# Kernel tuning notes

Hardware: AMD Instinct MI355X
Metric: run time of the kernel (lower is better)

## Reference

```python
import jax, jax.numpy as jnp
import numpy as np

NF, NLOC, NALL, NNEI = 2, 3072, 4096, 128
NTYPES, NSPLINE = 4, 1024
RCUT, RMIN, HH = 6.0, 0.0, 0.006
BOX = 20.0


def setup_inputs() -> dict:
    key = jax.random.key(0)
    k1, k2, k3, k4, k5 = jax.random.split(key, 5)
    extended_coord = jax.random.uniform(k1, (NF, NALL, 3), dtype=jnp.float32) * BOX
    extended_atype = jax.random.randint(k2, (NF, NALL), 0, NTYPES, dtype=jnp.int32)
    nlist = jax.random.randint(k3, (NF, NLOC, NNEI), 0, NALL, dtype=jnp.int32)
    # avoid self-neighbors (zero distance)
    self_idx = jnp.arange(NLOC, dtype=jnp.int32)[None, :, None]
    nlist = jnp.where(nlist == self_idx, (nlist + 1) % NALL, nlist)
    drop = jax.random.uniform(k4, (NF, NLOC, NNEI)) < 0.15
    nlist = jnp.where(drop, -1, nlist)
    tab_info = jnp.array([RMIN, HH, float(NSPLINE)], dtype=jnp.float32)
    tab_data = jax.random.normal(k5, (NTYPES, NTYPES, NSPLINE, 4), dtype=jnp.float32) * 0.1
    return {
        "extended_coord": extended_coord,
        "extended_atype": extended_atype,
        "nlist": nlist,
        "tab_info": tab_info,
        "tab_data": tab_data,
    }


def reference(extended_coord, extended_atype, nlist, tab_info, tab_data):
    nf, nloc, nnei = nlist.shape
    masked_nlist = jnp.clip(nlist, 0)
    # dense pairwise distances, as in the original module (nf, nall, nall)
    dr = extended_coord[:, :, None, :] - extended_coord[:, None, :, :]
    rr_full = jnp.sqrt(jnp.maximum(jnp.sum(dr * dr, axis=-1), 1e-30))
    # gather distances of listed neighbors (nf, nloc, nnei)
    rr = jnp.take_along_axis(rr_full[:, :nloc, :], masked_nlist, axis=2)
    i_type = extended_atype[:, :nloc]                                  # (nf, nloc)
    j_type = extended_atype[jnp.arange(nf)[:, None, None], masked_nlist]  # (nf, nloc, nnei)

    rmin = tab_info[0]
    hh = tab_info[1]
    uu = (rr - rmin) / hh
    uu = jnp.where(nlist != -1, uu, float(NSPLINE + 1))
    idx = uu.astype(jnp.int32)  # truncation toward zero, matches torch .to(int)
    uu = uu - idx

    # gather cubic-spline coefficients: (nf, nloc, nnei, 4)
    cidx = jnp.clip(idx, 0, NSPLINE - 1)
    coef = tab_data[i_type[:, :, None], j_type, cidx]
    coef = jnp.where((idx > NSPLINE)[..., None], 0.0, coef)

    a3, a2, a1, a0 = coef[..., 0], coef[..., 1], coef[..., 2], coef[..., 3]
    ener = ((a3 * uu + a2) * uu + a1) * uu + a0
    # zero beyond cutoff / beyond table range
    beyond = (rr >= RCUT) | (rr >= rmin + NSPLINE * hh)
    ener = jnp.where(beyond, 0.0, ener)
    # zero masked (padded) neighbor entries, then reduce over neighbors
    ener = jnp.where(nlist != -1, ener, 0.0)
    return 0.5 * jnp.sum(ener, axis=-1)  # (nf, nloc)
```

## Files before the change

kernel.cpp:

```cpp
#include <hip/hip_runtime.h>

#define NF      2
#define NLOC    3072
#define NALL    4096
#define NNEI    128
#define NTYPES  4
#define NSPLINE 1024

__device__ __forceinline__ float opaque(float x) {
    asm volatile("" : "+v"(x));
    return x;
}

__global__ __launch_bounds__(256) void pairtab_kernel(
    const float* __restrict__ coord,
    const int*   __restrict__ atype,
    const int*   __restrict__ nlist,
    const float* __restrict__ tab_info,
    const float* __restrict__ tab_data,
    float*       __restrict__ out)
{
    const int tid   = threadIdx.x;
    const int r     = tid >> 7;
    const int jj    = tid & 127;
    const int row   = blockIdx.x * 2 + r;

    const int f = (row >= NLOC) ? 1 : 0;
    const int i = row - f * NLOC;

    const float rmin = tab_info[0];
    const float hh   = tab_info[1];
    const float hi   = opaque((float)(1.0 / (double)hh));
    const float cut2 = opaque(opaque(1024.0f * hh) + rmin);

    const float* ci = coord + (size_t)(f * NALL + i) * 3;
    const float xi = ci[0], yi = ci[1], zi = ci[2];
    const int itype = atype[f * NALL + i];

    const int nj = nlist[(size_t)(f * NLOC + i) * NNEI + jj];
    const int mj = (nj < 0) ? 0 : nj;

    const float* cj = coord + (size_t)(f * NALL + mj) * 3;

    const float dx = opaque(xi - cj[0]);
    const float dy = opaque(yi - cj[1]);
    const float dz = opaque(zi - cj[2]);
    const float x2 = opaque(dx * dx);
    const float y2 = opaque(dy * dy);
    const float z2 = opaque(dz * dz);
    float ss = opaque(opaque(x2 + y2) + z2);
    ss = fmaxf(ss, 1e-30f);

    const float rr = (float)sqrt((double)ss);

    const float num = opaque(rr - rmin);
    float uu = opaque(num * hi);
    if (nj == -1) uu = (float)(NSPLINE + 1);

    const int idx = (int)uu;
    const float fu = opaque(uu - (float)idx);
    int cidx = idx;
    if (cidx < 0) cidx = 0;
    if (cidx > NSPLINE - 1) cidx = NSPLINE - 1;

    const int jtype = atype[f * NALL + mj];
    const float4 c4 = *(const float4*)(tab_data +
        ((size_t)((itype * NTYPES + jtype) * NSPLINE + cidx)) * 4);

    float a3 = c4.x, a2 = c4.y, a1 = c4.z, a0 = c4.w;
    if (idx > NSPLINE) { a3 = 0.f; a2 = 0.f; a1 = 0.f; a0 = 0.f; }

    float e = opaque(opaque(opaque(opaque(opaque(a3 * fu) + a2) * fu)
                            + a1) * fu) + a0;

    if (rr >= 6.0f || rr >= cut2 || nj == -1) e = 0.0f;

    double acc = (double)e;
    #pragma unroll
    for (int off = 32; off; off >>= 1)
        acc += __shfl_xor(acc, off);

    __shared__ double part[4];
    if ((tid & 63) == 0) part[tid >> 6] = acc;
    __syncthreads();
    if (jj == 0)
        out[row] = (float)(0.5 * (part[r * 2] + part[r * 2 + 1]));
}

extern "C" void kernel_launch(void* const* d_in, const int* in_sizes, int n_in,
                              void* d_out, int out_size, void* d_ws, size_t ws_size,
                              hipStream_t stream) {
    const float* coord    = (const float*)d_in[0];
    const int*   atype    = (const int*)  d_in[1];
    const int*   nlist    = (const int*)  d_in[2];
    const float* tab_info = (const float*)d_in[3];
    const float* tab_data = (const float*)d_in[4];
    float* out = (float*)d_out;

    const int blocks = (NF * NLOC) / 2;
    pairtab_kernel<<<blocks, 256, 0, stream>>>(coord, atype, nlist, tab_info,
                                               tab_data, out);
}
```

Measured before the change: 13.15 us.

## Stage frame coordinates and types in LDS, process eight rows per block

Each block now loads the entire frame's coordinates and atom types (4096 atoms packed as float4) into shared memory, then serves the random neighbor gathers from LDS instead of global memory. Blocks grow to 1024 threads covering 8 rows, and spline coefficient loads use nontemporal hints. The cost is that every block reloads 64KB of coordinates and types, 768 blocks in total, which adds global traffic and a full barrier before any useful work, and the large LDS footprint limits occupancy.

```diff
diff --git a/kernel.cpp b/kernel.cpp
--- a/kernel.cpp
+++ b/kernel.cpp
@@ -6,13 +6,16 @@
 #define NNEI    128
 #define NTYPES  4
 #define NSPLINE 1024
+#define RPB     8
+
+typedef float f32x4 __attribute__((ext_vector_type(4)));
 
 __device__ __forceinline__ float opaque(float x) {
     asm volatile("" : "+v"(x));
     return x;
 }
 
-__global__ __launch_bounds__(256) void pairtab_kernel(
+__global__ __launch_bounds__(1024) void pairtab_kernel(
     const float* __restrict__ coord,
     const int*   __restrict__ atype,
     const int*   __restrict__ nlist,
@@ -20,31 +23,51 @@
     const float* __restrict__ tab_data,
     float*       __restrict__ out)
 {
-    const int tid   = threadIdx.x;
-    const int r     = tid >> 7;
-    const int jj    = tid & 127;
-    const int row   = blockIdx.x * 2 + r;
+    __shared__ f32x4  atoms[NALL];
+    __shared__ double part[16];
+    float* ldsf = (float*)atoms;
 
-    const int f = (row >= NLOC) ? 1 : 0;
-    const int i = row - f * NLOC;
+    const int tid  = threadIdx.x;
+    const int row0 = blockIdx.x * RPB;
+    const int f    = (row0 >= NLOC) ? 1 : 0;
+
+    const float* cbase = coord + (size_t)f * NALL * 3;
+    #pragma unroll
+    for (int g = tid; g < NALL * 3; g += 1024) {
+        const float v = cbase[g];
+        const int a = g / 3;
+        const int comp = g - a * 3;
+        ldsf[a * 4 + comp] = v;
+    }
+    const int* tb = atype + (size_t)f * NALL;
+    #pragma unroll
+    for (int g = tid; g < NALL; g += 1024)
+        ldsf[g * 4 + 3] = __int_as_float(tb[g]);
+    __syncthreads();
+
+    const int rl   = tid >> 7;
+    const int jj   = tid & 127;
+    const int grow = row0 + rl;
+    const int i    = grow - f * NLOC;
 
     const float rmin = tab_info[0];
     const float hh   = tab_info[1];
     const float hi   = opaque((float)(1.0 / (double)hh));
     const float cut2 = opaque(opaque(1024.0f * hh) + rmin);
 
-    const float* ci = coord + (size_t)(f * NALL + i) * 3;
-    const float xi = ci[0], yi = ci[1], zi = ci[2];
-    const int itype = atype[f * NALL + i];
+    const f32x4 pi = atoms[i];
+    const float xi = pi.x, yi = pi.y, zi = pi.z;
+    const int itype = __float_as_int(pi.w);
 
-    const int nj = nlist[(size_t)(f * NLOC + i) * NNEI + jj];
+    const int nj = nlist[(size_t)grow * NNEI + jj];
     const int mj = (nj < 0) ? 0 : nj;
 
-    const float* cj = coord + (size_t)(f * NALL + mj) * 3;
+    const f32x4 pj = atoms[mj];
+    const int jtype = __float_as_int(pj.w);
 
-    const float dx = opaque(xi - cj[0]);
-    const float dy = opaque(yi - cj[1]);
-    const float dz = opaque(zi - cj[2]);
+    const float dx = opaque(xi - pj.x);
+    const float dy = opaque(yi - pj.y);
+    const float dz = opaque(zi - pj.z);
     const float x2 = opaque(dx * dx);
     const float y2 = opaque(dy * dy);
     const float z2 = opaque(dz * dz);
@@ -63,9 +86,9 @@
     if (cidx < 0) cidx = 0;
     if (cidx > NSPLINE - 1) cidx = NSPLINE - 1;
 
-    const int jtype = atype[f * NALL + mj];
-    const float4 c4 = *(const float4*)(tab_data +
-        ((size_t)((itype * NTYPES + jtype) * NSPLINE + cidx)) * 4);
+    const f32x4* tp = (const f32x4*)tab_data +
+        ((size_t)((itype * NTYPES + jtype) * NSPLINE + cidx));
+    const f32x4 c4 = __builtin_nontemporal_load(tp);
 
     float a3 = c4.x, a2 = c4.y, a1 = c4.z, a0 = c4.w;
     if (idx > NSPLINE) { a3 = 0.f; a2 = 0.f; a1 = 0.f; a0 = 0.f; }
@@ -80,11 +103,10 @@
     for (int off = 32; off; off >>= 1)
         acc += __shfl_xor(acc, off);
 
-    __shared__ double part[4];
     if ((tid & 63) == 0) part[tid >> 6] = acc;
     __syncthreads();
     if (jj == 0)
-        out[row] = (float)(0.5 * (part[r * 2] + part[r * 2 + 1]));
+        out[grow] = (float)(0.5 * (part[rl * 2] + part[rl * 2 + 1]));
 }
 
 extern "C" void kernel_launch(void* const* d_in, const int* in_sizes, int n_in,
@@ -97,7 +119,7 @@
     const float* tab_data = (const float*)d_in[4];
     float* out = (float*)d_out;
 
-    const int blocks = (NF * NLOC) / 2;
-    pairtab_kernel<<<blocks, 256, 0, stream>>>(coord, atype, nlist, tab_info,
-                                               tab_data, out);
+    const int blocks = (NF * NLOC) / RPB;
+    pairtab_kernel<<<blocks, 1024, 0, stream>>>(coord, atype, nlist, tab_info,
+                                                tab_data, out);
 }
```

New measurement: 13.10 us, median of 2. About the same (-0.4%).
